# Performance work log

Measured on AMD Instinct MI355X. Metric: run time of the kernel, lower is better.

Reference implementation:

```python
import jax, jax.numpy as jnp
import numpy as np

T_PRED = 30   # max_pred_time * hz
B = 2048      # number of trajectory segments (batch)
D = 256       # n_hidden_after_deconv
DH = 128      # n_hidden_after_deconv / 2


def setup_inputs() -> dict:
    key = jax.random.key(0)
    k1, k2, k3, k4 = jax.random.split(key, 4)
    return {
        "encode_samples": jax.random.normal(k1, (T_PRED, B, D), dtype=jnp.float32),
        "representation_cur": jax.random.normal(k2, (B, DH), dtype=jnp.float32),
        "Wk_w": jax.random.normal(k3, (T_PRED, D, DH), dtype=jnp.float32) * (1.0 / np.sqrt(DH)),
        "Wk_b": jax.random.normal(k4, (T_PRED, D), dtype=jnp.float32) * 0.01,
    }


def reference(encode_samples, representation_cur, Wk_w, Wk_b):
    # encode_samples: [T, B, D] future encoder outputs (c_{t+i})
    # Wk_w: [T, D, DH] per-step Linear weights (torch layout [out,in]); Wk_b: [T, D]
    T, Bn, Dd = encode_samples.shape
    # pred[i] = Wk[i](representation_cur)  -> [T, B, D]
    pred = jnp.einsum('bh,tdh->tbd', representation_cur, Wk_w) + Wk_b[:, None, :]
    # total_i = encode_samples[i] @ pred[i].T  -> [T, B, B]
    totals = jnp.einsum('tbd,tcd->tbc', encode_samples, pred)
    # nce += sum(diag(log_softmax(total, dim=1))) per step (torch LogSoftmax default dim=1 on 2D)
    logp = jax.nn.log_softmax(totals, axis=2)
    nce = jnp.sum(jnp.diagonal(logp, axis1=1, axis2=2))
    calc_step = Bn * T  # all pred_steps > T-1 (all segments long enough)
    nce = nce / (-1.0 * calc_step)
    # accuracy from the LAST step (matches the original loop-carried `correct`/`batch_idx`)
    probs = jax.nn.softmax(totals[-1], axis=1)          # softmax over dim=1
    correct = jnp.sum(jnp.argmax(probs, axis=0) == jnp.arange(Bn))  # argmax over dim=0
    accuracy = correct.astype(jnp.float32) / Bn
    return (accuracy, nce, jnp.asarray(Bn), jnp.asarray(calc_step))
```

## Files before the change

### kernel.cpp

```cpp
#include <hip/hip_runtime.h>
#include <math.h>

typedef unsigned short u16;
typedef unsigned int   u32;
typedef unsigned long long u64;

#define T_PRED 30
#define BN 2048
#define DD 256
#define DHH 128
#define ESHIFT 64.0f

typedef __attribute__((ext_vector_type(8))) short short8;
typedef __attribute__((ext_vector_type(4))) float f32x4;

#if defined(__has_builtin)
#if __has_builtin(__builtin_amdgcn_exp2f)
#define EXPSH(v) __builtin_amdgcn_exp2f(__builtin_fmaf((v), 1.44269504f, -92.3324826f))
#endif
#endif
#ifndef EXPSH
#define EXPSH(v) __expf((v) - ESHIFT)
#endif

#define WS_S      4096
#define WS_TABLE  (WS_S + 245760)
#define WS_ZEND   (WS_TABLE + 16384)
#define WS_WH     WS_ZEND
#define WS_WL     (WS_WH + 1966080)
#define WS_RH     (WS_WL + 1966080)
#define WS_RL     (WS_RH + 524288)
#define WS_GH     (WS_RL + 524288)
#define WS_GL29   (WS_GH + 15728640)
#define WS_T29    (WS_GL29 + 524288)

__device__ __forceinline__ u16 bf16_rne(float f) {
    u32 u = __float_as_uint(f);
    u32 r = u + 0x7fffu + ((u >> 16) & 1u);
    return (u16)(r >> 16);
}

__device__ __forceinline__ short8 pack_hi8(const float* f) {
    short8 r;
#pragma unroll
    for (int k = 0; k < 8; ++k) r[k] = (short)(u16)(__float_as_uint(f[k]) >> 16);
    return r;
}
__device__ __forceinline__ short8 pack_lo8(const float* f) {
    short8 r;
#pragma unroll
    for (int k = 0; k < 8; ++k) {
        float hf = __uint_as_float(__float_as_uint(f[k]) & 0xffff0000u);
        r[k] = (short)bf16_rne(f[k] - hf);
    }
    return r;
}

#define AS1 __attribute__((address_space(1)))
#define AS3 __attribute__((address_space(3)))

__global__ __launch_bounds__(256) void prep_kernel(
    const float* __restrict__ rep, const float* __restrict__ Ww,
    u16* __restrict__ Rh, u16* __restrict__ Rl,
    u16* __restrict__ Wh, u16* __restrict__ Wl, u32* __restrict__ wsz)
{
    const int bx = blockIdx.x, tid = threadIdx.x;
    for (int i = bx * 256 + tid; i < 66560; i += 32768) wsz[i] = 0;

    if (bx < 120) {
        __shared__ float tile[64][132];
        const int t = bx >> 2, d0 = (bx & 3) * 64;
        for (int it = 0; it < 8; ++it) {
            int idx = tid + it * 256;
            int row = idx >> 5, off = (idx & 31) * 4;
            *(float4*)&tile[row][off] =
                *(const float4*)&Ww[((size_t)t * DD + d0 + row) * DHH + off];
        }
        __syncthreads();
        const int h = tid >> 1, half = tid & 1;
        const bool lo = (t == T_PRED - 1);
        for (int d4 = 0; d4 < 32; d4 += 4) {
            ushort4 hv, lv;
            u16* hp = (u16*)&hv; u16* lp = (u16*)&lv;
#pragma unroll
            for (int k = 0; k < 4; ++k) {
                float v = tile[half * 32 + d4 + k][h];
                u16 hb = bf16_rne(v);
                hp[k] = hb;
                float hf = __uint_as_float((u32)hb << 16);
                lp[k] = bf16_rne(v - hf);
            }
            size_t o = (size_t)t * DHH * DD + (size_t)h * DD + d0 + half * 32 + d4;
            *(ushort4*)&Wh[o] = hv;
            if (lo) *(ushort4*)&Wl[o] = lv;
        }
    } else {
        int base = (bx - 120) * 256 + tid;
        for (int p = 0; p < 32; ++p) {
            int i = base + p * 2048;
            float4 v = ((const float4*)rep)[i];
            float vv[4] = {v.x, v.y, v.z, v.w};
            u16 h[4], l[4];
#pragma unroll
            for (int k = 0; k < 4; ++k) {
                h[k] = bf16_rne(vv[k]);
                float hf = __uint_as_float((u32)h[k] << 16);
                l[k] = bf16_rne(vv[k] - hf);
            }
            ((ushort4*)Rh)[i] = make_ushort4(h[0], h[1], h[2], h[3]);
            ((ushort4*)Rl)[i] = make_ushort4(l[0], l[1], l[2], l[3]);
        }
    }
}

__global__ __launch_bounds__(256) void g_fused_kernel(
    const float* __restrict__ E, const u16* __restrict__ Wh,
    const u16* __restrict__ Wl, u16* __restrict__ Gh,
    u16* __restrict__ Gh29, u16* __restrict__ Gl29)
{
    __shared__ __attribute__((aligned(16))) u32 esm[2][4096];
    __shared__ __attribute__((aligned(16))) u16 wsm[2][4096];
    const int y    = blockIdx.y;
    const int tid  = threadIdx.x;
    const int lane = tid & 63;
    const int w    = tid >> 6;
    const int ml   = lane & 15;
    const int quad = lane >> 4;

    if (y < 29) {
        const int t    = y;
        const int row0 = blockIdx.x * 128;
        const int wr   = (w >> 1) * 64;
        const int wc   = (w & 1) * 64;
        const float* Et = E + (size_t)t * BN * DD;
        const u16*   Wt = Wh + (size_t)t * DHH * DD;
        const int erow_l = lane >> 3, eunit = lane & 7;
        const int wcol_l = lane >> 2, wunit = lane & 3;

        auto stage = [&](int buf, int kc) {
#pragma unroll
            for (int n = 0; n < 4; ++n) {
                int q = w * 4 + n;
                int row = q * 8 + erow_l;
                int unit = (eunit - row) & 7;
                const float* g = Et + (size_t)(row0 + row) * DD + kc * 32 + unit * 4;
                __builtin_amdgcn_global_load_lds((const AS1 u32*)g,
                    (AS3 u32*)(&esm[buf][q * 256]), 16, 0, 0);
            }
#pragma unroll
            for (int n = 0; n < 2; ++n) {
                int q = w * 2 + n;
                int col = q * 16 + wcol_l;
                int unit = (wunit - col) & 3;
                const u16* g = Wt + (size_t)col * DD + kc * 32 + unit * 8;
                __builtin_amdgcn_global_load_lds((const AS1 u32*)g,
                    (AS3 u32*)(&wsm[buf][q * 512]), 16, 0, 0);
            }
        };

        f32x4 acc[4][4];
#pragma unroll
        for (int i = 0; i < 4; ++i)
#pragma unroll
            for (int j = 0; j < 4; ++j) acc[i][j] = (f32x4){0.f, 0.f, 0.f, 0.f};

        stage(0, 0);
        __syncthreads();
#pragma unroll 1
        for (int kc = 0; kc < 8; ++kc) {
            if (kc < 7) stage((kc + 1) & 1, kc + 1);
            const int pb = kc & 1;
            short8 ah[4], bh[4];
#pragma unroll
            for (int i = 0; i < 4; ++i) {
                int row = wr + i * 16 + ml;
                float4 f0 = *(const float4*)&esm[pb][row * 32 + (((quad * 2 + 0 + row) & 7) * 4)];
                float4 f1 = *(const float4*)&esm[pb][row * 32 + (((quad * 2 + 1 + row) & 7) * 4)];
                float f[8] = {f0.x, f0.y, f0.z, f0.w, f1.x, f1.y, f1.z, f1.w};
                ah[i] = pack_hi8(f);
            }
#pragma unroll
            for (int j = 0; j < 4; ++j) {
                int col = wc + j * 16 + ml;
                bh[j] = *(const short8*)&wsm[pb][col * 32 + ((quad + col) & 3) * 8];
            }
#pragma unroll
            for (int i = 0; i < 4; ++i)
#pragma unroll
                for (int j = 0; j < 4; ++j)
                    acc[i][j] = __builtin_amdgcn_mfma_f32_16x16x32_bf16(ah[i], bh[j], acc[i][j], 0, 0, 0);
            __syncthreads();
        }

#pragma unroll
        for (int i = 0; i < 4; ++i)
#pragma unroll
            for (int j = 0; j < 4; ++j)
#pragma unroll
                for (int r = 0; r < 4; ++r) {
                    int row = row0 + wr + i * 16 + quad * 4 + r;
                    int col = wc + j * 16 + ml;
                    Gh[((size_t)t * BN + row) * DHH + col] = bf16_rne(acc[i][j][r]);
                }
    } else {
        const int row0 = ((y - 29) * 16 + blockIdx.x) * 32;
        const int wc   = w * 32;
        const size_t tE = (size_t)(T_PRED - 1) * BN * DD;
        const size_t tW = (size_t)(T_PRED - 1) * DHH * DD;

#pragma unroll 1
        for (int rr = 0; rr < 32; rr += 16) {
            f32x4 acc[2];
            acc[0] = (f32x4){0.f, 0.f, 0.f, 0.f};
            acc[1] = (f32x4){0.f, 0.f, 0.f, 0.f};
#pragma unroll
            for (int kc = 0; kc < 8; ++kc) {
                const float* ep = E + tE + (size_t)(row0 + rr + ml) * DD + kc * 32 + quad * 8;
                float4 e0 = *(const float4*)ep;
                float4 e1 = *(const float4*)(ep + 4);
                float f[8] = {e0.x, e0.y, e0.z, e0.w, e1.x, e1.y, e1.z, e1.w};
                short8 ah = pack_hi8(f);
                short8 al = pack_lo8(f);
#pragma unroll
                for (int j = 0; j < 2; ++j) {
                    size_t o = tW + (size_t)(wc + j * 16 + ml) * DD + kc * 32 + quad * 8;
                    short8 bh = *(const short8*)(Wh + o);
                    short8 bl = *(const short8*)(Wl + o);
                    acc[j] = __builtin_amdgcn_mfma_f32_16x16x32_bf16(ah, bh, acc[j], 0, 0, 0);
                    acc[j] = __builtin_amdgcn_mfma_f32_16x16x32_bf16(ah, bl, acc[j], 0, 0, 0);
                    acc[j] = __builtin_amdgcn_mfma_f32_16x16x32_bf16(al, bh, acc[j], 0, 0, 0);
                }
            }
#pragma unroll
            for (int j = 0; j < 2; ++j)
#pragma unroll
                for (int r = 0; r < 4; ++r) {
                    int row = row0 + rr + quad * 4 + r;
                    int col = wc + j * 16 + ml;
                    float v = acc[j][r];
                    u16 hb = bf16_rne(v);
                    float hf = __uint_as_float((u32)hb << 16);
                    Gh29[(size_t)row * DHH + col] = hb;
                    Gl29[(size_t)row * DHH + col] = bf16_rne(v - hf);
                }
        }
    }
}

__global__ __launch_bounds__(512, 4) void nce_fused_kernel(
    const u16* __restrict__ Gh, const u16* __restrict__ Gh29,
    const u16* __restrict__ Gl29, const u16* __restrict__ Rh,
    const u16* __restrict__ Rl, float* __restrict__ S,
    float* __restrict__ tot29, float* __restrict__ nce_acc)
{
    __shared__ __attribute__((aligned(16))) u16 sm[32768];
    const int z    = blockIdx.z;
    const int tid  = threadIdx.x;
    const int lane = tid & 63;
    const int w    = tid >> 6;
    const int ml   = lane & 15;
    const int quad = lane >> 4;
    float* S29 = S + (size_t)(T_PRED - 1) * BN;

    if (z < 29) {
        const int t  = z;
        const int c0 = (int)blockIdx.y << 8;
        const int r0 = (int)blockIdx.x << 8;

#pragma unroll
        for (int n = 0; n < 8; ++n) {
            const int q   = (w << 3) + n;
            const int U   = (q << 6) | lane;
            const int col = U >> 4;
            const int g   = ((U & 15) - col) & 15;
            const u16* src = Rh + (size_t)(c0 + col) * DHH + g * 8;
            __builtin_amdgcn_global_load_lds((const AS1 u32*)src,
                (AS3 u32*)(&sm[q << 9]), 16, 0, 0);
        }

        short8 ah[2][4];
#pragma unroll
        for (int i = 0; i < 2; ++i)
#pragma unroll
            for (int kc = 0; kc < 4; ++kc)
                ah[i][kc] = *(const short8*)(Gh +
                    ((size_t)t * BN + r0 + (w << 5) + (i << 4) + ml) * DHH
                    + (kc << 5) + (quad << 3));

        float ssum[2][4];
#pragma unroll
        for (int i = 0; i < 2; ++i)
#pragma unroll
            for (int r = 0; r < 4; ++r) ssum[i][r] = 0.f;
        float dsum = 0.f;
        const bool dblk = (c0 == r0);
        const int rbase = r0 + (w << 5) + (quad << 2);

        __syncthreads();

#pragma unroll 2
        for (int ch = 0; ch < 8; ++ch) {
            f32x4 acc[2][2];
#pragma unroll
            for (int i = 0; i < 2; ++i)
#pragma unroll
                for (int j = 0; j < 2; ++j) acc[i][j] = (f32x4){0.f, 0.f, 0.f, 0.f};

#pragma unroll
            for (int kc = 0; kc < 4; ++kc) {
                const int slot = ((kc << 2) + quad + ml) & 15;
                const short8 bh0 = *(const short8*)&sm[((ch << 5) + ml) * 128 + (slot << 3)];
                const short8 bh1 = *(const short8*)&sm[((ch << 5) + 16 + ml) * 128 + (slot << 3)];
                acc[0][0] = __builtin_amdgcn_mfma_f32_16x16x32_bf16(ah[0][kc], bh0, acc[0][0], 0, 0, 0);
                acc[0][1] = __builtin_amdgcn_mfma_f32_16x16x32_bf16(ah[0][kc], bh1, acc[0][1], 0, 0, 0);
                acc[1][0] = __builtin_amdgcn_mfma_f32_16x16x32_bf16(ah[1][kc], bh0, acc[1][0], 0, 0, 0);
                acc[1][1] = __builtin_amdgcn_mfma_f32_16x16x32_bf16(ah[1][kc], bh1, acc[1][1], 0, 0, 0);
            }

#pragma unroll
            for (int i = 0; i < 2; ++i)
#pragma unroll
                for (int r = 0; r < 4; ++r) {
                    float e0 = EXPSH(acc[i][0][r]);
                    float e1 = EXPSH(acc[i][1][r]);
                    ssum[i][r] += e0 + e1;
                }
            if (dblk && ch == w) {
#pragma unroll
                for (int r = 0; r < 4; ++r)
                    if (ml == (quad << 2) + r)
                        dsum += acc[0][0][r] + acc[1][1][r];
            }
        }

#pragma unroll
        for (int i = 0; i < 2; ++i)
#pragma unroll
            for (int r = 0; r < 4; ++r) {
                float v = ssum[i][r];
#pragma unroll
                for (int o = 1; o < 16; o <<= 1) v += __shfl_xor(v, o, 64);
                if (ml == 0)
                    atomicAdd(S + (size_t)t * BN + rbase + (i << 4) + r, v);
            }
        if (dblk) {
            float dv = dsum;
#pragma unroll
            for (int o = 1; o < 64; o <<= 1) dv += __shfl_xor(dv, o, 64);
            if (lane == 0) atomicAdd(nce_acc, -dv);
        }
    } else {
        const int idx = ((z - 29) << 6) + ((int)blockIdx.y << 3) + (int)blockIdx.x;
        const int rb  = idx >> 4, cb = idx & 15;
        const int r0  = rb << 7, c0 = cb << 7;
        const bool dblk = (rb == cb);

#pragma unroll
        for (int n = 0; n < 8; ++n) {
            const int q    = (w << 3) + n;
            const int U    = (q << 6) | lane;
            const int colL = (U >> 4) & 127;
            const int half = U >> 11;
            const int g    = ((U & 15) - colL) & 15;
            const u16* src = (half ? Rl : Rh) + (size_t)(c0 + colL) * DHH + g * 8;
            __builtin_amdgcn_global_load_lds((const AS1 u32*)src,
                (AS3 u32*)(&sm[q << 9]), 16, 0, 0);
        }

        short8 ah[4], al[4];
#pragma unroll
        for (int kc = 0; kc < 4; ++kc) {
            size_t o = (size_t)(r0 + (w << 4) + ml) * DHH + (kc << 5) + (quad << 3);
            ah[kc] = *(const short8*)(Gh29 + o);
            al[kc] = *(const short8*)(Gl29 + o);
        }

        float esum[4];
#pragma unroll
        for (int r = 0; r < 4; ++r) esum[r] = 0.f;
        float dsum = 0.f;
        const int rbase = r0 + (w << 4) + (quad << 2);

        __syncthreads();

#pragma unroll
        for (int ch = 0; ch < 4; ++ch) {
            f32x4 acc[2];
            acc[0] = (f32x4){0.f, 0.f, 0.f, 0.f};
            acc[1] = (f32x4){0.f, 0.f, 0.f, 0.f};
#pragma unroll
            for (int kc = 0; kc < 4; ++kc) {
                const int slot = ((kc << 2) + quad + ml) & 15;
                const int i0 = ((ch << 5) + ml) * 128 + (slot << 3);
                const int i1 = i0 + 16 * 128;
                const short8 bh0 = *(const short8*)&sm[i0];
                const short8 bl0 = *(const short8*)&sm[16384 + i0];
                const short8 bh1 = *(const short8*)&sm[i1];
                const short8 bl1 = *(const short8*)&sm[16384 + i1];
                acc[0] = __builtin_amdgcn_mfma_f32_16x16x32_bf16(ah[kc], bh0, acc[0], 0, 0, 0);
                acc[0] = __builtin_amdgcn_mfma_f32_16x16x32_bf16(ah[kc], bl0, acc[0], 0, 0, 0);
                acc[0] = __builtin_amdgcn_mfma_f32_16x16x32_bf16(al[kc], bh0, acc[0], 0, 0, 0);
                acc[1] = __builtin_amdgcn_mfma_f32_16x16x32_bf16(ah[kc], bh1, acc[1], 0, 0, 0);
                acc[1] = __builtin_amdgcn_mfma_f32_16x16x32_bf16(ah[kc], bl1, acc[1], 0, 0, 0);
                acc[1] = __builtin_amdgcn_mfma_f32_16x16x32_bf16(al[kc], bh1, acc[1], 0, 0, 0);
            }

#pragma unroll
            for (int j = 0; j < 2; ++j)
#pragma unroll
                for (int r = 0; r < 4; ++r) {
                    float v = acc[j][r];
                    int row = rbase + r;
                    int col = c0 + (ch << 5) + (j << 4) + ml;
                    tot29[(size_t)row * BN + col] = v;
                    esum[r] += EXPSH(v);
                }
            if (dblk && ch == (w >> 1)) {
#pragma unroll
                for (int r = 0; r < 4; ++r)
                    if (ml == (quad << 2) + r)
                        dsum += (w & 1) ? acc[1][r] : acc[0][r];
            }
        }

#pragma unroll
        for (int r = 0; r < 4; ++r) {
            float v = esum[r];
#pragma unroll
            for (int o = 1; o < 16; o <<= 1) v += __shfl_xor(v, o, 64);
            if (ml == 0) atomicAdd(S29 + rbase + r, v);
        }
        if (dblk) {
            float dv = dsum;
#pragma unroll
            for (int o = 1; o < 64; o <<= 1) dv += __shfl_xor(dv, o, 64);
            if (lane == 0) atomicAdd(nce_acc, -dv);
        }
    }
}

__device__ __forceinline__ u32 fenc(float f) {
    u32 u = __float_as_uint(f);
    return (u & 0x80000000u) ? ~u : (u | 0x80000000u);
}

__global__ __launch_bounds__(256) void argmax_fin_kernel(
    const float* __restrict__ tot29, const float* __restrict__ S,
    u64* __restrict__ table, u32* __restrict__ done,
    float* __restrict__ nce_acc, float* __restrict__ out)
{
    __shared__ float lse_s[128];
    __shared__ float part[4];
    __shared__ u32 lastflag;
    __shared__ int cpart[4];
    const int tid = threadIdx.x;
    const int c   = blockIdx.x * 256 + tid;
    const int b0  = blockIdx.y * 128;
    const float* S29 = S + (size_t)(T_PRED - 1) * BN;

    {
        const int base = ((int)blockIdx.y * 8 + (int)blockIdx.x) * 480;
        float v = 0.f;
        for (int i = tid; i < 480; i += 256)
            v += ESHIFT + __logf(S[base + i]);
#pragma unroll
        for (int o = 1; o < 64; o <<= 1) v += __shfl_xor(v, o, 64);
        if ((tid & 63) == 0) part[tid >> 6] = v;
        __syncthreads();
        if (tid == 0)
            atomicAdd(nce_acc, part[0] + part[1] + part[2] + part[3]);
    }

    if (tid < 128) lse_s[tid] = ESHIFT + __logf(S29[b0 + tid]);
    __syncthreads();

    float best = -3.4e38f; int bi = 0;
    for (int b = 0; b < 128; ++b) {
        float v = tot29[(size_t)(b0 + b) * BN + c] - lse_s[b];
        if (v > best) { best = v; bi = b0 + b; }
    }
    u64 key = ((u64)fenc(best) << 32) | (u32)(0xFFFFFFFFu - (u32)bi);
    atomicMax(table + c, key);

    __threadfence();
    if (tid == 0) lastflag = (atomicAdd(done, 1u) == 127u);
    __syncthreads();
    if (!lastflag) return;

    int cnt = 0;
    for (int i = tid; i < BN; i += 256) {
        u64 k = atomicAdd(table + i, 0ull);
        u32 b = 0xFFFFFFFFu - (u32)(k & 0xFFFFFFFFull);
        if ((int)b == i) cnt++;
    }
#pragma unroll
    for (int o = 1; o < 64; o <<= 1) cnt += __shfl_xor(cnt, o, 64);
    if ((tid & 63) == 0) cpart[tid >> 6] = cnt;
    __syncthreads();
    if (tid == 0) {
        int correct = cpart[0] + cpart[1] + cpart[2] + cpart[3];
        float nce = atomicAdd(nce_acc, 0.0f);
        out[0] = (float)correct / (float)BN;
        out[1] = nce / (float)(BN * T_PRED);
        out[2] = (float)BN;
        out[3] = (float)(BN * T_PRED);
    }
}

extern "C" void kernel_launch(void* const* d_in, const int* in_sizes, int n_in,
                              void* d_out, int out_size, void* d_ws, size_t ws_size,
                              hipStream_t stream) {
    const float* E   = (const float*)d_in[0];
    const float* rep = (const float*)d_in[1];
    const float* Ww  = (const float*)d_in[2];
    float* out = (float*)d_out;

    char* ws = (char*)d_ws;
    float* nce_acc = (float*)(ws + 0);
    u32*   done    = (u32*)(ws + 8);
    float* S       = (float*)(ws + WS_S);
    u64*   table   = (u64*)(ws + WS_TABLE);
    u16*   Wh      = (u16*)(ws + WS_WH);
    u16*   Wl      = (u16*)(ws + WS_WL);
    u16*   Rh      = (u16*)(ws + WS_RH);
    u16*   Rl      = (u16*)(ws + WS_RL);
    u16*   Gh      = (u16*)(ws + WS_GH);
    u16*   Gh29    = Gh + (size_t)(T_PRED - 1) * BN * DHH;
    u16*   Gl29    = (u16*)(ws + WS_GL29);
    float* tot29   = (float*)(ws + WS_T29);

    prep_kernel<<<dim3(128), 256, 0, stream>>>(rep, Ww, Rh, Rl, Wh, Wl, (u32*)ws);
    g_fused_kernel<<<dim3(16, 33), 256, 0, stream>>>(E, Wh, Wl, Gh, Gh29, Gl29);
    nce_fused_kernel<<<dim3(8, 8, 33), 512, 0, stream>>>(Gh, Gh29, Gl29, Rh, Rl,
                                                         S, tot29, nce_acc);
    argmax_fin_kernel<<<dim3(8, 16), 256, 0, stream>>>(tot29, S, table, done,
                                                       nce_acc, out);
}
```

Measured before the change: 186.6 us.

## Restructure G projection kernel to stage full K tiles in LDS with 512 threads

The G = E·W projection kernel now uses 512-thread blocks that load the whole 128x256 E tile (converted to bf16 while staging) and the whole W tile into one 128KB shared buffer in a single pass. This replaces the double-buffered 8-step K loop. Each wave then holds all its A fragments in registers and iterates over 8 column tiles, and the last-step split-precision path is reshaped to 16 blocks of 128 rows. This removes per-chunk barriers and the repeated fp32 unpacking, but it drops the overlap between loads and MFMAs. It also uses a large LDS allocation, which limits occupancy to about one block per CU.

```diff
diff --git a/kernel.cpp b/kernel.cpp
--- a/kernel.cpp
+++ b/kernel.cpp
@@ -113,137 +113,122 @@
     }
 }
 
-__global__ __launch_bounds__(256) void g_fused_kernel(
+__global__ __launch_bounds__(512, 2) void g_fused_kernel(
     const float* __restrict__ E, const u16* __restrict__ Wh,
     const u16* __restrict__ Wl, u16* __restrict__ Gh,
     u16* __restrict__ Gh29, u16* __restrict__ Gl29)
 {
-    __shared__ __attribute__((aligned(16))) u32 esm[2][4096];
-    __shared__ __attribute__((aligned(16))) u16 wsm[2][4096];
+    __shared__ __attribute__((aligned(16))) u16 sm[65536];
     const int y    = blockIdx.y;
+    const int bx   = blockIdx.x;
     const int tid  = threadIdx.x;
     const int lane = tid & 63;
     const int w    = tid >> 6;
     const int ml   = lane & 15;
     const int quad = lane >> 4;
+    const int r0   = bx << 7;
 
     if (y < 29) {
-        const int t    = y;
-        const int row0 = blockIdx.x * 128;
-        const int wr   = (w >> 1) * 64;
-        const int wc   = (w & 1) * 64;
+        const int t = y;
         const float* Et = E + (size_t)t * BN * DD;
         const u16*   Wt = Wh + (size_t)t * DHH * DD;
-        const int erow_l = lane >> 3, eunit = lane & 7;
-        const int wcol_l = lane >> 2, wunit = lane & 3;
-
-        auto stage = [&](int buf, int kc) {
-#pragma unroll
-            for (int n = 0; n < 4; ++n) {
-                int q = w * 4 + n;
-                int row = q * 8 + erow_l;
-                int unit = (eunit - row) & 7;
-                const float* g = Et + (size_t)(row0 + row) * DD + kc * 32 + unit * 4;
-                __builtin_amdgcn_global_load_lds((const AS1 u32*)g,
-                    (AS3 u32*)(&esm[buf][q * 256]), 16, 0, 0);
-            }
-#pragma unroll
-            for (int n = 0; n < 2; ++n) {
-                int q = w * 2 + n;
-                int col = q * 16 + wcol_l;
-                int unit = (wunit - col) & 3;
-                const u16* g = Wt + (size_t)col * DD + kc * 32 + unit * 8;
-                __builtin_amdgcn_global_load_lds((const AS1 u32*)g,
-                    (AS3 u32*)(&wsm[buf][q * 512]), 16, 0, 0);
-            }
-        };
-
-        f32x4 acc[4][4];
-#pragma unroll
-        for (int i = 0; i < 4; ++i)
-#pragma unroll
-            for (int j = 0; j < 4; ++j) acc[i][j] = (f32x4){0.f, 0.f, 0.f, 0.f};
-
-        stage(0, 0);
+
+#pragma unroll
+        for (int n = 0; n < 8; ++n) {
+            const int q    = (w << 3) + n;
+            const int U    = (q << 6) | lane;
+            const int col  = U >> 5;
+            const int g    = ((U & 31) - 2 * col) & 31;
+            const u16* src = Wt + (size_t)col * DD + g * 8;
+            __builtin_amdgcn_global_load_lds((const AS1 u32*)src,
+                (AS3 u32*)(&sm[32768 + (q << 9)]), 16, 0, 0);
+        }
+#pragma unroll
+        for (int k = 0; k < 16; ++k) {
+            const int idx  = tid + (k << 9);
+            const int row  = idx >> 6;
+            const int col4 = idx & 63;
+            float4 v = *(const float4*)(Et + (size_t)(r0 + row) * DD + (col4 << 2));
+            ushort4 h;
+            h.x = (u16)(__float_as_uint(v.x) >> 16);
+            h.y = (u16)(__float_as_uint(v.y) >> 16);
+            h.z = (u16)(__float_as_uint(v.z) >> 16);
+            h.w = (u16)(__float_as_uint(v.w) >> 16);
+            const int slot = ((col4 >> 1) + 2 * row) & 31;
+            *(ushort4*)&sm[(row << 8) + (slot << 3) + ((col4 & 1) << 2)] = h;
+        }
+
         __syncthreads();
+
+        short8 ah[8];
+#pragma unroll
+        for (int kc = 0; kc < 8; ++kc) {
+            const int row  = (w << 4) + ml;
+            const int slot = ((kc << 2) + quad + 2 * row) & 31;
+            ah[kc] = *(const short8*)&sm[(row << 8) + (slot << 3)];
+        }
+        f32x4 acc[8];
+#pragma unroll
+        for (int j = 0; j < 8; ++j) acc[j] = (f32x4){0.f, 0.f, 0.f, 0.f};
+
 #pragma unroll 1
         for (int kc = 0; kc < 8; ++kc) {
-            if (kc < 7) stage((kc + 1) & 1, kc + 1);
-            const int pb = kc & 1;
-            short8 ah[4], bh[4];
-#pragma unroll
-            for (int i = 0; i < 4; ++i) {
-                int row = wr + i * 16 + ml;
-                float4 f0 = *(const float4*)&esm[pb][row * 32 + (((quad * 2 + 0 + row) & 7) * 4)];
-                float4 f1 = *(const float4*)&esm[pb][row * 32 + (((quad * 2 + 1 + row) & 7) * 4)];
-                float f[8] = {f0.x, f0.y, f0.z, f0.w, f1.x, f1.y, f1.z, f1.w};
-                ah[i] = pack_hi8(f);
-            }
-#pragma unroll
-            for (int j = 0; j < 4; ++j) {
-                int col = wc + j * 16 + ml;
-                bh[j] = *(const short8*)&wsm[pb][col * 32 + ((quad + col) & 3) * 8];
-            }
-#pragma unroll
-            for (int i = 0; i < 4; ++i)
-#pragma unroll
-                for (int j = 0; j < 4; ++j)
-                    acc[i][j] = __builtin_amdgcn_mfma_f32_16x16x32_bf16(ah[i], bh[j], acc[i][j], 0, 0, 0);
-            __syncthreads();
-        }
-
-#pragma unroll
-        for (int i = 0; i < 4; ++i)
-#pragma unroll
-            for (int j = 0; j < 4; ++j)
-#pragma unroll
-                for (int r = 0; r < 4; ++r) {
-                    int row = row0 + wr + i * 16 + quad * 4 + r;
-                    int col = wc + j * 16 + ml;
-                    Gh[((size_t)t * BN + row) * DHH + col] = bf16_rne(acc[i][j][r]);
-                }
+#pragma unroll
+            for (int j = 0; j < 8; ++j) {
+                const int col  = (j << 4) + ml;
+                const int slot = ((kc << 2) + quad + 2 * col) & 31;
+                const short8 bh = *(const short8*)&sm[32768 + (col << 8) + (slot << 3)];
+                acc[j] = __builtin_amdgcn_mfma_f32_16x16x32_bf16(ah[kc], bh, acc[j], 0, 0, 0);
+            }
+        }
+
+#pragma unroll
+        for (int j = 0; j < 8; ++j)
+#pragma unroll
+            for (int r = 0; r < 4; ++r) {
+                const int row = r0 + (w << 4) + (quad << 2) + r;
+                Gh[((size_t)t * BN + row) * DHH + (j << 4) + ml] = bf16_rne(acc[j][r]);
+            }
     } else {
-        const int row0 = ((y - 29) * 16 + blockIdx.x) * 32;
-        const int wc   = w * 32;
         const size_t tE = (size_t)(T_PRED - 1) * BN * DD;
         const size_t tW = (size_t)(T_PRED - 1) * DHH * DD;
 
+        f32x4 acc[8];
+#pragma unroll
+        for (int j = 0; j < 8; ++j) acc[j] = (f32x4){0.f, 0.f, 0.f, 0.f};
+
 #pragma unroll 1
-        for (int rr = 0; rr < 32; rr += 16) {
-            f32x4 acc[2];
-            acc[0] = (f32x4){0.f, 0.f, 0.f, 0.f};
-            acc[1] = (f32x4){0.f, 0.f, 0.f, 0.f};
-#pragma unroll
-            for (int kc = 0; kc < 8; ++kc) {
-                const float* ep = E + tE + (size_t)(row0 + rr + ml) * DD + kc * 32 + quad * 8;
-                float4 e0 = *(const float4*)ep;
-                float4 e1 = *(const float4*)(ep + 4);
-                float f[8] = {e0.x, e0.y, e0.z, e0.w, e1.x, e1.y, e1.z, e1.w};
-                short8 ah = pack_hi8(f);
-                short8 al = pack_lo8(f);
-#pragma unroll
-                for (int j = 0; j < 2; ++j) {
-                    size_t o = tW + (size_t)(wc + j * 16 + ml) * DD + kc * 32 + quad * 8;
-                    short8 bh = *(const short8*)(Wh + o);
-                    short8 bl = *(const short8*)(Wl + o);
-                    acc[j] = __builtin_amdgcn_mfma_f32_16x16x32_bf16(ah, bh, acc[j], 0, 0, 0);
-                    acc[j] = __builtin_amdgcn_mfma_f32_16x16x32_bf16(ah, bl, acc[j], 0, 0, 0);
-                    acc[j] = __builtin_amdgcn_mfma_f32_16x16x32_bf16(al, bh, acc[j], 0, 0, 0);
-                }
-            }
-#pragma unroll
-            for (int j = 0; j < 2; ++j)
-#pragma unroll
-                for (int r = 0; r < 4; ++r) {
-                    int row = row0 + rr + quad * 4 + r;
-                    int col = wc + j * 16 + ml;
-                    float v = acc[j][r];
-                    u16 hb = bf16_rne(v);
-                    float hf = __uint_as_float((u32)hb << 16);
-                    Gh29[(size_t)row * DHH + col] = hb;
-                    Gl29[(size_t)row * DHH + col] = bf16_rne(v - hf);
-                }
-        }
+        for (int kc = 0; kc < 8; ++kc) {
+            const float* ep = E + tE + (size_t)(r0 + (w << 4) + ml) * DD
+                              + (kc << 5) + (quad << 3);
+            float4 e0 = *(const float4*)ep;
+            float4 e1 = *(const float4*)(ep + 4);
+            float f[8] = {e0.x, e0.y, e0.z, e0.w, e1.x, e1.y, e1.z, e1.w};
+            short8 ahh = pack_hi8(f);
+            short8 all = pack_lo8(f);
+#pragma unroll
+            for (int j = 0; j < 8; ++j) {
+                size_t o = tW + (size_t)((j << 4) + ml) * DD + (kc << 5) + (quad << 3);
+                short8 bh = *(const short8*)(Wh + o);
+                short8 bl = *(const short8*)(Wl + o);
+                acc[j] = __builtin_amdgcn_mfma_f32_16x16x32_bf16(ahh, bh, acc[j], 0, 0, 0);
+                acc[j] = __builtin_amdgcn_mfma_f32_16x16x32_bf16(ahh, bl, acc[j], 0, 0, 0);
+                acc[j] = __builtin_amdgcn_mfma_f32_16x16x32_bf16(all, bh, acc[j], 0, 0, 0);
+            }
+        }
+
+#pragma unroll
+        for (int j = 0; j < 8; ++j)
+#pragma unroll
+            for (int r = 0; r < 4; ++r) {
+                const int row = r0 + (w << 4) + (quad << 2) + r;
+                const int col = (j << 4) + ml;
+                float v = acc[j][r];
+                u16 hb = bf16_rne(v);
+                float hf = __uint_as_float((u32)hb << 16);
+                Gh29[(size_t)row * DHH + col] = hb;
+                Gl29[(size_t)row * DHH + col] = bf16_rne(v - hf);
+            }
     }
 }
 
@@ -530,7 +515,7 @@
     float* tot29   = (float*)(ws + WS_T29);
 
     prep_kernel<<<dim3(128), 256, 0, stream>>>(rep, Ww, Rh, Rl, Wh, Wl, (u32*)ws);
-    g_fused_kernel<<<dim3(16, 33), 256, 0, stream>>>(E, Wh, Wl, Gh, Gh29, Gl29);
+    g_fused_kernel<<<dim3(16, 30), 512, 0, stream>>>(E, Wh, Wl, Gh, Gh29, Gl29);
     nce_fused_kernel<<<dim3(8, 8, 33), 512, 0, stream>>>(Gh, Gh29, Gl29, Rh, Rl,
                                                          S, tot29, nce_acc);
     argmax_fin_kernel<<<dim3(8, 16), 256, 0, stream>>>(tot29, S, table, done,
```

Result: slower. 293.9 us (+57.5%).
